# Performance work log

Hardware: AMD Instinct MI355X
Metric: run time of the kernel (lower is better)

Reference implementation:

```python
import jax, jax.numpy as jnp
import numpy as np

N_NODES = 50000
N_EDGES = 1600000


def _gcn_conv(x, src, dst, W, b, num_nodes):
    # PyG GCNConv: out = D^-1/2 (A + I) D^-1/2 (x W) + b
    h = x @ W  # transform first (in_channels >= out_channels)
    deg = jax.ops.segment_sum(jnp.ones_like(dst, dtype=h.dtype), dst,
                              num_segments=num_nodes)
    dinv = jax.lax.rsqrt(deg)  # deg >= 1 thanks to self-loops
    norm = dinv[src] * dinv[dst]  # [E+N]
    msg = h[src] * norm[:, None]  # gather + scale
    out = jax.ops.segment_sum(msg, dst, num_segments=num_nodes)
    return out + b


def setup_inputs() -> dict:
    key = jax.random.key(0)
    k1, k2, k3, k4 = jax.random.split(key, 4)
    x = jax.random.normal(k1, (N_NODES, 512), dtype=jnp.float32)
    edge_index = jax.random.randint(k2, (2, N_EDGES), 0, N_NODES, dtype=jnp.int64)
    # Glorot-ish init for the two GCNConv weights
    W1 = jax.random.normal(k3, (512, 128), dtype=jnp.float32) * (1.0 / np.sqrt(512))
    b1 = jnp.zeros((128,), dtype=jnp.float32)
    W2 = jax.random.normal(k4, (128, 64), dtype=jnp.float32) * (1.0 / np.sqrt(128))
    b2 = jnp.zeros((64,), dtype=jnp.float32)
    return {"x": x, "edge_index": edge_index, "W1": W1, "b1": b1,
            "W2": W2, "b2": b2}


def reference(x, edge_index, W1, b1, W2, b2):
    num_nodes = x.shape[0]
    loop = jnp.arange(num_nodes, dtype=edge_index.dtype)
    src = jnp.concatenate([edge_index[0], loop])  # add self-loops
    dst = jnp.concatenate([edge_index[1], loop])
    h = jax.nn.relu(_gcn_conv(x, src, dst, W1, b1, num_nodes))
    out = _gcn_conv(h, src, dst, W2, b2, num_nodes)
    return out
```

## Files before the change

### kernel.cpp

```cpp
#include <hip/hip_runtime.h>
#include <hip/hip_bf16.h>


typedef __attribute__((ext_vector_type(8))) short short8;
typedef __attribute__((ext_vector_type(4))) float f32x4;

#define BSHIFT 9
#define BSIZE 512
constexpr int NBMAX = 128;
constexpr int CAP = 32768;
constexpr int CHUNK = 4096;

__device__ __forceinline__ unsigned short bf16_bits(float f) {
  __hip_bfloat16 h = __float2bfloat16(f);
  return *(unsigned short*)&h;
}
__device__ __forceinline__ float bf16_f(unsigned short u) {
  __hip_bfloat16 h = *(__hip_bfloat16*)&u;
  return __bfloat162float(h);
}
__device__ __forceinline__ void gload_lds16(const void* g, void* l) {
  __builtin_amdgcn_global_load_lds(
      (const __attribute__((address_space(1))) unsigned*)g,
      (__attribute__((address_space(3))) unsigned*)l, 16, 0, 0);
}
__device__ __forceinline__ int edge_at(const void* p, long long i, int is64) {
  return is64 ? (int)((const long long*)p)[i] : ((const int*)p)[i];
}

__global__ __launch_bounds__(256) void k_binA(
    const void* __restrict__ eidx, int* __restrict__ ccur,
    unsigned* __restrict__ pairs,
    const float* __restrict__ W1, unsigned short* __restrict__ W1h,
    unsigned short* __restrict__ W1l,
    const float* __restrict__ W2, unsigned short* __restrict__ W2h,
    unsigned short* __restrict__ W2l, int E, int NB, int nchunks) {
  const int tid = threadIdx.x;
  if ((int)blockIdx.x >= nchunks) {
    int o = ((int)blockIdx.x - nchunks) * 256 + tid;
    const float* W; unsigned short *Wh, *Wl; int K, Nn;
    if (o < 512 * 128) { W = W1; Wh = W1h; Wl = W1l; K = 512; Nn = 128; }
    else { o -= 512 * 128; if (o >= 128 * 64) return;
           W = W2; Wh = W2h; Wl = W2l; K = 128; Nn = 64; }
    int n = o / K, k = o % K;
    float w = W[(long long)k * Nn + n];
    unsigned short hb = bf16_bits(w);
    Wh[o] = hb;
    Wl[o] = bf16_bits(w - bf16_f(hb));
    return;
  }
  __shared__ int s_nz;
  __shared__ int cnt[NBMAX];
  __shared__ int scn[NBMAX + 1];
  __shared__ int cur[NBMAX];
  __shared__ int gbase[NBMAX];
  __shared__ unsigned out[CHUNK];
  if (tid == 0) s_nz = 0;
  for (int b = tid; b < NBMAX; b += 256) cnt[b] = 0;
  __syncthreads();
  {
    int nz = 0;
    for (int i = 1 + 2 * tid; i < 4096; i += 512)
      nz |= (((const int*)eidx)[i] != 0);
    if (nz) atomicOr(&s_nz, 1);
  }
  __syncthreads();
  const int is64 = (s_nz == 0) ? 1 : 0;
  const int cs = blockIdx.x * CHUNK;
  const int n = min(CHUNK, E - cs);
  unsigned pk[CHUNK / 256];
#pragma unroll
  for (int it = 0; it < CHUNK / 256; ++it) {
    int i = cs + it * 256 + tid;
    unsigned p = 0xFFFFFFFFu;
    if (i < E) {
      int s = edge_at(eidx, i, is64);
      int d = edge_at(eidx, (long long)E + i, is64);
      p = ((unsigned)d << 16) | (unsigned)s;
      atomicAdd(&cnt[d >> BSHIFT], 1);
    }
    pk[it] = p;
  }
  __syncthreads();
  if (tid < NB) scn[tid + 1] = cnt[tid];
  if (tid == 0) scn[0] = 0;
  __syncthreads();
  for (int off = 1; off < NB; off <<= 1) {
    int t = 0;
    if (tid < NB && tid + 1 > off) t = scn[tid + 1 - off];
    __syncthreads();
    if (tid < NB && tid + 1 > off) scn[tid + 1] += t;
    __syncthreads();
  }
  if (tid < NB) {
    cur[tid] = scn[tid];
    gbase[tid] = (cnt[tid] > 0)
        ? (tid * CAP + atomicAdd(&ccur[tid], cnt[tid])) : 0;
  }
  __syncthreads();
#pragma unroll
  for (int it = 0; it < CHUNK / 256; ++it) {
    unsigned p = pk[it];
    if (p != 0xFFFFFFFFu) {
      int b = (int)(p >> (16 + BSHIFT));
      int pos = atomicAdd(&cur[b], 1);
      out[pos] = p;
    }
  }
  __syncthreads();
  for (int p2 = tid; p2 < n; p2 += 256) {
    unsigned v = out[p2];
    int b = (int)(v >> (16 + BSHIFT));
    pairs[gbase[b] + (p2 - scn[b])] = v;
  }
}

__global__ __launch_bounds__(256) void k_binB(
    const unsigned* __restrict__ pairs, const int* __restrict__ ccur,
    int* __restrict__ rowptr, float* __restrict__ dinv,
    unsigned short* __restrict__ elist, int N, int NB, int E) {
  __shared__ int scn2[NBMAX];
  __shared__ int hist[BSIZE];
  __shared__ int loc[BSIZE];
  const int b = blockIdx.x;
  const int tid = threadIdx.x;
  if (b == 0 && tid == 0) rowptr[N] = E;
  if (tid < NBMAX) scn2[tid] = (tid < NB) ? ccur[tid] : 0;
  __syncthreads();
  for (int off = 1; off < NBMAX; off <<= 1) {
    int t = (tid < NBMAX && tid >= off) ? scn2[tid - off] : 0;
    __syncthreads();
    if (tid < NBMAX) scn2[tid] += t;
    __syncthreads();
  }
  const int cntb = ccur[b];
  const int base = scn2[b] - cntb;
  const int nbeg = b * CAP;
  const int j0 = tid, j1 = tid + 256;
  hist[j0] = 0; hist[j1] = 0;
  __syncthreads();
  for (int i = tid; i < cntb; i += 256) {
    unsigned v = pairs[nbeg + i];
    atomicAdd(&hist[(v >> 16) & (BSIZE - 1)], 1);
  }
  __syncthreads();
  loc[j0] = hist[j0]; loc[j1] = hist[j1];
  __syncthreads();
  for (int off = 1; off < BSIZE; off <<= 1) {
    int v0 = (j0 >= off) ? loc[j0 - off] : 0;
    int v1 = (j1 >= off) ? loc[j1 - off] : 0;
    __syncthreads();
    loc[j0] += v0; loc[j1] += v1;
    __syncthreads();
  }
  int c0 = base + loc[j0] - hist[j0];
  int c1 = base + loc[j1] - hist[j1];
  int gd0 = b * BSIZE + j0, gd1 = b * BSIZE + j1;
  if (gd0 < N) { rowptr[gd0] = c0; dinv[gd0] = rsqrtf((float)(hist[j0] + 1)); }
  if (gd1 < N) { rowptr[gd1] = c1; dinv[gd1] = rsqrtf((float)(hist[j1] + 1)); }
  __syncthreads();
  hist[j0] = c0; hist[j1] = c1;
  __syncthreads();
  for (int i = tid; i < cntb; i += 256) {
    unsigned v = pairs[nbeg + i];
    int pos = atomicAdd(&hist[(v >> 16) & (BSIZE - 1)], 1);
    elist[pos] = (unsigned short)(v & 0xFFFFu);
  }
}

template <int K, int NOUT, int WM, int WY, int WX>
__global__ __launch_bounds__(256) void k_gemm_mfma(
    const float* __restrict__ X, const unsigned short* __restrict__ Whi,
    const unsigned short* __restrict__ Wlo, const float* __restrict__ dinv,
    unsigned short* __restrict__ Hs, int M) {
  constexpr int BM = WM * WY;
  constexpr int BN = 64 * WX;
  constexpr int KC = 32;
  constexpr int I = WM / 16;
  static_assert(WY * WX == 4, "4 waves");
  static_assert(BN == NOUT, "block covers full N");
  __shared__ unsigned short Ah[BM][KC], Al[BM][KC];
  __shared__ unsigned short Bh[BN][KC], Bl[BN][KC];
  const int tid = threadIdx.x;
  const int lane = tid & 63, wv = tid >> 6;
  const int wy = wv / WX, wx = wv % WX;
  const int fm = lane & 15;
  const int fq = lane >> 4;
  const int base = blockIdx.x * BM;

  f32x4 acc[I][4];
#pragma unroll
  for (int i = 0; i < I; ++i)
#pragma unroll
    for (int j = 0; j < 4; ++j) acc[i][j] = (f32x4){0.f, 0.f, 0.f, 0.f};

  for (int k0 = 0; k0 < K; k0 += KC) {
    __syncthreads();
#pragma unroll
    for (int it = 0; it < BM / 32; ++it) {
      int chunk = tid + it * 256;
      int r = chunk >> 3, c = chunk & 7;
      float4 v = make_float4(0.f, 0.f, 0.f, 0.f);
      if (base + r < M) v = *(const float4*)&X[(long long)(base + r) * K + k0 + c * 4];
      ushort4 hv, lv;
      hv.x = bf16_bits(v.x); lv.x = bf16_bits(v.x - bf16_f(hv.x));
      hv.y = bf16_bits(v.y); lv.y = bf16_bits(v.y - bf16_f(hv.y));
      hv.z = bf16_bits(v.z); lv.z = bf16_bits(v.z - bf16_f(hv.z));
      hv.w = bf16_bits(v.w); lv.w = bf16_bits(v.w - bf16_f(hv.w));
      *(ushort4*)&Ah[r][c * 4] = hv;
      *(ushort4*)&Al[r][c * 4] = lv;
    }
#pragma unroll
    for (int it = 0; it < (BN * 4) / 256; ++it) {
      int cb = it * 256 + wv * 64;
      int chunk = cb + lane;
      int n = chunk >> 2, cc = chunk & 3;
      const long long go = (long long)n * K + k0 + cc * 8;
      gload_lds16(&Whi[go], (unsigned short*)Bh + (size_t)cb * 8);
      gload_lds16(&Wlo[go], (unsigned short*)Bl + (size_t)cb * 8);
    }
    __syncthreads();
    short8 ah[I], al[I], bh[4], bl[4];
#pragma unroll
    for (int i = 0; i < I; ++i) {
      ah[i] = *(short8*)&Ah[wy * WM + i * 16 + fm][fq * 8];
      al[i] = *(short8*)&Al[wy * WM + i * 16 + fm][fq * 8];
    }
#pragma unroll
    for (int j = 0; j < 4; ++j) {
      bh[j] = *(short8*)&Bh[wx * 64 + j * 16 + fm][fq * 8];
      bl[j] = *(short8*)&Bl[wx * 64 + j * 16 + fm][fq * 8];
    }
#pragma unroll
    for (int i = 0; i < I; ++i)
#pragma unroll
      for (int j = 0; j < 4; ++j) {
        acc[i][j] = __builtin_amdgcn_mfma_f32_16x16x32_bf16(ah[i], bh[j], acc[i][j], 0, 0, 0);
        acc[i][j] = __builtin_amdgcn_mfma_f32_16x16x32_bf16(ah[i], bl[j], acc[i][j], 0, 0, 0);
        acc[i][j] = __builtin_amdgcn_mfma_f32_16x16x32_bf16(al[i], bh[j], acc[i][j], 0, 0, 0);
      }
  }
#pragma unroll
  for (int i = 0; i < I; ++i) {
#pragma unroll
    for (int reg = 0; reg < 4; ++reg) {
      int row = base + wy * WM + i * 16 + fq * 4 + reg;
      if (row < M) {
        float dv = dinv[row];
#pragma unroll
        for (int j = 0; j < 4; ++j)
          Hs[(long long)row * NOUT + wx * 64 + j * 16 + fm] =
              bf16_bits(acc[i][j][reg] * dv);
      }
    }
  }
}

__device__ __forceinline__ void acc8(float* a, uint4 u) {
  const unsigned* p = (const unsigned*)&u;
#pragma unroll
  for (int q = 0; q < 4; ++q) {
    unsigned w = p[q];
    a[2 * q]     += __uint_as_float(w << 16);
    a[2 * q + 1] += __uint_as_float(w & 0xFFFF0000u);
  }
}

template <int C, bool RELU>
__global__ __launch_bounds__(256) void k_gather(
    const int* __restrict__ rowptr, const unsigned short* __restrict__ elist,
    const float* __restrict__ dinv, const unsigned short* __restrict__ Hs,
    const float* __restrict__ bias, float* __restrict__ OUT, int N) {
  constexpr int TPN = C / 8;
  constexpr int NPB = 256 / TPN;
  const int node = blockIdx.x * NPB + (int)threadIdx.x / TPN;
  const int lane = (int)threadIdx.x % TPN;
  if (node >= N) return;
  const int col = lane * 8;
  const int beg = rowptr[node];
  const int end = rowptr[node + 1];
  float a0[8] = {0, 0, 0, 0, 0, 0, 0, 0};
  float a1[8] = {0, 0, 0, 0, 0, 0, 0, 0};
  acc8(a0, *(const uint4*)&Hs[(long long)node * C + col]);
  int e = beg;
  for (; e + 3 < end; e += 4) {
    int s0 = elist[e], s1 = elist[e + 1], s2 = elist[e + 2], s3 = elist[e + 3];
    uint4 v0 = *(const uint4*)&Hs[(long long)s0 * C + col];
    uint4 v1 = *(const uint4*)&Hs[(long long)s1 * C + col];
    uint4 v2 = *(const uint4*)&Hs[(long long)s2 * C + col];
    uint4 v3 = *(const uint4*)&Hs[(long long)s3 * C + col];
    acc8(a0, v0); acc8(a1, v1); acc8(a0, v2); acc8(a1, v3);
  }
  for (; e < end; ++e) {
    uint4 v0 = *(const uint4*)&Hs[(long long)elist[e] * C + col];
    acc8(a0, v0);
  }
  const float dv = dinv[node];
  float o[8];
#pragma unroll
  for (int i = 0; i < 8; ++i) {
    o[i] = (a0[i] + a1[i]) * dv + bias[col + i];
    if (RELU) o[i] = fmaxf(o[i], 0.f);
  }
  *(float4*)&OUT[(long long)node * C + col] = make_float4(o[0], o[1], o[2], o[3]);
  *(float4*)&OUT[(long long)node * C + col + 4] = make_float4(o[4], o[5], o[6], o[7]);
}

extern "C" void kernel_launch(void* const* d_in, const int* in_sizes, int n_in,
                              void* d_out, int out_size, void* d_ws, size_t ws_size,
                              hipStream_t stream) {
  const float* x  = (const float*)d_in[0];
  const void*  ei = d_in[1];
  const float* W1 = (const float*)d_in[2];
  const float* b1 = (const float*)d_in[3];
  const float* W2 = (const float*)d_in[4];
  const float* b2 = (const float*)d_in[5];
  float* out = (float*)d_out;
  const int N = in_sizes[0] / 512;
  const int E = in_sizes[1] / 2;
  const int NB = (N + BSIZE - 1) >> BSHIFT;
  const int nchunks = (E + CHUNK - 1) / CHUNK;

  char* ws = (char*)d_ws;
  size_t off = 0;
  auto take = [&](size_t bytes) {
    void* p = ws + off;
    off = (off + bytes + 255) & ~(size_t)255;
    return p;
  };
  float* dinv   = (float*)take((size_t)N * 4);
  int*   rowptr = (int*)take((size_t)(N + 1) * 4);
  int*   ccur   = (int*)take((size_t)NBMAX * 4);
  unsigned short* elist = (unsigned short*)take((size_t)E * 2);
  unsigned short* Wt1h = (unsigned short*)take((size_t)512 * 128 * 2);
  unsigned short* Wt1l = (unsigned short*)take((size_t)512 * 128 * 2);
  unsigned short* Wt2h = (unsigned short*)take((size_t)128 * 64 * 2);
  unsigned short* Wt2l = (unsigned short*)take((size_t)128 * 64 * 2);
  unsigned short* Hs = (unsigned short*)take((size_t)N * 128 * 2);
  float* h2     = (float*)take((size_t)N * 128 * 4);
  unsigned short* Hs2 = Hs;
  unsigned* pairs = (unsigned*)h2;

  const int B = 256;
  constexpr int WJOBS = (512 * 128 + 128 * 64) / 256;
  hipMemsetAsync(ccur, 0, (size_t)NBMAX * 4, stream);
  k_binA<<<nchunks + WJOBS, B, 0, stream>>>(ei, ccur, pairs,
                                            W1, Wt1h, Wt1l, W2, Wt2h, Wt2l,
                                            E, NB, nchunks);
  k_binB<<<NB, B, 0, stream>>>(pairs, ccur, rowptr, dinv, elist, N, NB, E);
  k_gemm_mfma<512, 128, 32, 2, 2><<<(N + 63) / 64, B, 0, stream>>>(
      x, Wt1h, Wt1l, dinv, Hs, N);
  k_gather<128, true><<<(N + 15) / 16, B, 0, stream>>>(rowptr, elist, dinv, Hs, b1, h2, N);
  k_gemm_mfma<128, 64, 32, 4, 1><<<(N + 127) / 128, B, 0, stream>>>(
      h2, Wt2h, Wt2l, dinv, Hs2, N);
  k_gather<64, false><<<(N + 31) / 32, B, 0, stream>>>(rowptr, elist, dinv, Hs2, b2, out, N);
}
```

Before: 338.7 us.

## Double-buffer LDS tiles in MFMA GEMM and shrink second GEMM tile

Restructures the split-bf16 MFMA GEMM so that LDS holds two buffers. The next K-chunk's A values are loaded into registers and its B tiles issued via global_load_lds while the current chunk is computed, which needs one barrier per iteration instead of two. The second GEMM's per-wave M tile also shrinks from 32 to 16 rows, doubling its block count for more parallelism. The cost is twice the LDS and extra registers for the prefetched A values, and the overlap is only safe if the async LDS loads have completed by the barrier.

```diff
diff --git a/kernel.cpp b/kernel.cpp
--- a/kernel.cpp
+++ b/kernel.cpp
@@ -177,16 +177,20 @@
   constexpr int BN = 64 * WX;
   constexpr int KC = 32;
   constexpr int I = WM / 16;
+  constexpr int NK = K / KC;
+  constexpr int AIT = BM / 32;
+  constexpr int BIT = (BN * 4) / 256;
   static_assert(WY * WX == 4, "4 waves");
   static_assert(BN == NOUT, "block covers full N");
-  __shared__ unsigned short Ah[BM][KC], Al[BM][KC];
-  __shared__ unsigned short Bh[BN][KC], Bl[BN][KC];
+  __shared__ unsigned short Ah[2][BM][KC], Al[2][BM][KC];
+  __shared__ unsigned short Bh[2][BN][KC], Bl[2][BN][KC];
   const int tid = threadIdx.x;
   const int lane = tid & 63, wv = tid >> 6;
   const int wy = wv / WX, wx = wv % WX;
   const int fm = lane & 15;
   const int fq = lane >> 4;
   const int base = blockIdx.x * BM;
+  const int ar = tid >> 3, ac = tid & 7;
 
   f32x4 acc[I][4];
 #pragma unroll
@@ -194,42 +198,52 @@
 #pragma unroll
     for (int j = 0; j < 4; ++j) acc[i][j] = (f32x4){0.f, 0.f, 0.f, 0.f};
 
-  for (int k0 = 0; k0 < K; k0 += KC) {
-    __syncthreads();
-#pragma unroll
-    for (int it = 0; it < BM / 32; ++it) {
-      int chunk = tid + it * 256;
-      int r = chunk >> 3, c = chunk & 7;
-      float4 v = make_float4(0.f, 0.f, 0.f, 0.f);
-      if (base + r < M) v = *(const float4*)&X[(long long)(base + r) * K + k0 + c * 4];
+  float4 av[AIT];
+
+  auto loadA = [&](int k0) {
+#pragma unroll
+    for (int it = 0; it < AIT; ++it) {
+      int r = ar + it * 32;
+      av[it] = make_float4(0.f, 0.f, 0.f, 0.f);
+      if (base + r < M)
+        av[it] = *(const float4*)&X[(long long)(base + r) * K + k0 + ac * 4];
+    }
+  };
+  auto writeA = [&](int buf) {
+#pragma unroll
+    for (int it = 0; it < AIT; ++it) {
+      int r = ar + it * 32;
       ushort4 hv, lv;
-      hv.x = bf16_bits(v.x); lv.x = bf16_bits(v.x - bf16_f(hv.x));
-      hv.y = bf16_bits(v.y); lv.y = bf16_bits(v.y - bf16_f(hv.y));
-      hv.z = bf16_bits(v.z); lv.z = bf16_bits(v.z - bf16_f(hv.z));
-      hv.w = bf16_bits(v.w); lv.w = bf16_bits(v.w - bf16_f(hv.w));
-      *(ushort4*)&Ah[r][c * 4] = hv;
-      *(ushort4*)&Al[r][c * 4] = lv;
-    }
-#pragma unroll
-    for (int it = 0; it < (BN * 4) / 256; ++it) {
+      hv.x = bf16_bits(av[it].x); lv.x = bf16_bits(av[it].x - bf16_f(hv.x));
+      hv.y = bf16_bits(av[it].y); lv.y = bf16_bits(av[it].y - bf16_f(hv.y));
+      hv.z = bf16_bits(av[it].z); lv.z = bf16_bits(av[it].z - bf16_f(hv.z));
+      hv.w = bf16_bits(av[it].w); lv.w = bf16_bits(av[it].w - bf16_f(hv.w));
+      *(ushort4*)&Ah[buf][r][ac * 4] = hv;
+      *(ushort4*)&Al[buf][r][ac * 4] = lv;
+    }
+  };
+  auto issueB = [&](int k0, int buf) {
+#pragma unroll
+    for (int it = 0; it < BIT; ++it) {
       int cb = it * 256 + wv * 64;
       int chunk = cb + lane;
       int n = chunk >> 2, cc = chunk & 3;
       const long long go = (long long)n * K + k0 + cc * 8;
-      gload_lds16(&Whi[go], (unsigned short*)Bh + (size_t)cb * 8);
-      gload_lds16(&Wlo[go], (unsigned short*)Bl + (size_t)cb * 8);
-    }
-    __syncthreads();
+      gload_lds16(&Whi[go], (unsigned short*)&Bh[buf][0][0] + (size_t)cb * 8);
+      gload_lds16(&Wlo[go], (unsigned short*)&Bl[buf][0][0] + (size_t)cb * 8);
+    }
+  };
+  auto compute = [&](int buf) {
     short8 ah[I], al[I], bh[4], bl[4];
 #pragma unroll
     for (int i = 0; i < I; ++i) {
-      ah[i] = *(short8*)&Ah[wy * WM + i * 16 + fm][fq * 8];
-      al[i] = *(short8*)&Al[wy * WM + i * 16 + fm][fq * 8];
+      ah[i] = *(short8*)&Ah[buf][wy * WM + i * 16 + fm][fq * 8];
+      al[i] = *(short8*)&Al[buf][wy * WM + i * 16 + fm][fq * 8];
     }
 #pragma unroll
     for (int j = 0; j < 4; ++j) {
-      bh[j] = *(short8*)&Bh[wx * 64 + j * 16 + fm][fq * 8];
-      bl[j] = *(short8*)&Bl[wx * 64 + j * 16 + fm][fq * 8];
+      bh[j] = *(short8*)&Bh[buf][wx * 64 + j * 16 + fm][fq * 8];
+      bl[j] = *(short8*)&Bl[buf][wx * 64 + j * 16 + fm][fq * 8];
     }
 #pragma unroll
     for (int i = 0; i < I; ++i)
@@ -239,7 +253,23 @@
         acc[i][j] = __builtin_amdgcn_mfma_f32_16x16x32_bf16(ah[i], bl[j], acc[i][j], 0, 0, 0);
         acc[i][j] = __builtin_amdgcn_mfma_f32_16x16x32_bf16(al[i], bh[j], acc[i][j], 0, 0, 0);
       }
-  }
+  };
+
+  loadA(0);
+  issueB(0, 0);
+  writeA(0);
+  __syncthreads();
+  int cur = 0;
+  for (int t = 0; t < NK - 1; ++t) {
+    loadA((t + 1) * KC);
+    issueB((t + 1) * KC, cur ^ 1);
+    compute(cur);
+    writeA(cur ^ 1);
+    __syncthreads();
+    cur ^= 1;
+  }
+  compute(cur);
+
 #pragma unroll
   for (int i = 0; i < I; ++i) {
 #pragma unroll
@@ -351,7 +381,7 @@
   k_gemm_mfma<512, 128, 32, 2, 2><<<(N + 63) / 64, B, 0, stream>>>(
       x, Wt1h, Wt1l, dinv, Hs, N);
   k_gather<128, true><<<(N + 15) / 16, B, 0, stream>>>(rowptr, elist, dinv, Hs, b1, h2, N);
-  k_gemm_mfma<128, 64, 32, 4, 1><<<(N + 127) / 128, B, 0, stream>>>(
+  k_gemm_mfma<128, 64, 16, 4, 1><<<(N + 63) / 64, B, 0, stream>>>(
       h2, Wt2h, Wt2l, dinv, Hs2, N);
   k_gather<64, false><<<(N + 31) / 32, B, 0, stream>>>(rowptr, elist, dinv, Hs2, b2, out, N);
 }
```

Result: no change. 336.3 us (-0.7%).

## Double-buffer GEMM tiles, load A directly to registers, pre-swizzle weights

Applied to the files above, without the earlier changes.

The MFMA GEMM now loads X rows straight into registers in the MFMA fragment layout and converts them to bf16 hi/lo in registers, which removes the A tile in LDS. The weight tiles are prepacked in fragment order by k_binA and double-buffered in LDS, with the next tile's loads issued before the current tile's MFMAs. This is meant to hide global load latency and cut LDS traffic and barriers. The second GEMM also moves to smaller 64-row blocks for more parallelism. In exchange, register pressure rises from keeping two A buffers in flight.

```diff
diff --git a/kernel.cpp b/kernel.cpp
--- a/kernel.cpp
+++ b/kernel.cpp
@@ -38,11 +38,19 @@
   const int tid = threadIdx.x;
   if ((int)blockIdx.x >= nchunks) {
     int o = ((int)blockIdx.x - nchunks) * 256 + tid;
-    const float* W; unsigned short *Wh, *Wl; int K, Nn;
-    if (o < 512 * 128) { W = W1; Wh = W1h; Wl = W1l; K = 512; Nn = 128; }
+    const float* W; unsigned short *Wh, *Wl; int Nn;
+    if (o < 512 * 128) { W = W1; Wh = W1h; Wl = W1l; Nn = 128; }
     else { o -= 512 * 128; if (o >= 128 * 64) return;
-           W = W2; Wh = W2h; Wl = W2l; K = 128; Nn = 64; }
-    int n = o / K, k = o % K;
+           W = W2; Wh = W2h; Wl = W2l; Nn = 64; }
+    int e = o & 7;
+    int fm = (o >> 3) & 15;
+    int fq = (o >> 7) & 3;
+    int rest = o >> 9;
+    int nt16 = Nn >> 4;
+    int jt = rest % nt16;
+    int t = rest / nt16;
+    int k = t * 32 + fq * 8 + e;
+    int n = jt * 16 + fm;
     float w = W[(long long)k * Nn + n];
     unsigned short hb = bf16_bits(w);
     Wh[o] = hb;
@@ -177,10 +185,11 @@
   constexpr int BN = 64 * WX;
   constexpr int KC = 32;
   constexpr int I = WM / 16;
+  constexpr int NK = K / KC;
+  constexpr int BIT = BN / 64;
   static_assert(WY * WX == 4, "4 waves");
   static_assert(BN == NOUT, "block covers full N");
-  __shared__ unsigned short Ah[BM][KC], Al[BM][KC];
-  __shared__ unsigned short Bh[BN][KC], Bl[BN][KC];
+  __shared__ unsigned short Bh[2][BN * KC], Bl[2][BN * KC];
   const int tid = threadIdx.x;
   const int lane = tid & 63, wv = tid >> 6;
   const int wy = wv / WX, wx = wv % WX;
@@ -194,42 +203,64 @@
 #pragma unroll
     for (int j = 0; j < 4; ++j) acc[i][j] = (f32x4){0.f, 0.f, 0.f, 0.f};
 
-  for (int k0 = 0; k0 < K; k0 += KC) {
-    __syncthreads();
-#pragma unroll
-    for (int it = 0; it < BM / 32; ++it) {
-      int chunk = tid + it * 256;
-      int r = chunk >> 3, c = chunk & 7;
-      float4 v = make_float4(0.f, 0.f, 0.f, 0.f);
-      if (base + r < M) v = *(const float4*)&X[(long long)(base + r) * K + k0 + c * 4];
-      ushort4 hv, lv;
-      hv.x = bf16_bits(v.x); lv.x = bf16_bits(v.x - bf16_f(hv.x));
-      hv.y = bf16_bits(v.y); lv.y = bf16_bits(v.y - bf16_f(hv.y));
-      hv.z = bf16_bits(v.z); lv.z = bf16_bits(v.z - bf16_f(hv.z));
-      hv.w = bf16_bits(v.w); lv.w = bf16_bits(v.w - bf16_f(hv.w));
-      *(ushort4*)&Ah[r][c * 4] = hv;
-      *(ushort4*)&Al[r][c * 4] = lv;
-    }
-#pragma unroll
-    for (int it = 0; it < (BN * 4) / 256; ++it) {
+  float4 av[2][I][2];
+
+  auto loadA = [&](int k0, int pb) {
+#pragma unroll
+    for (int i = 0; i < I; ++i) {
+      int row = base + wy * WM + i * 16 + fm;
+      av[pb][i][0] = make_float4(0.f, 0.f, 0.f, 0.f);
+      av[pb][i][1] = make_float4(0.f, 0.f, 0.f, 0.f);
+      if (row < M) {
+        const float4* p = (const float4*)&X[(long long)row * K + k0 + fq * 8];
+        av[pb][i][0] = p[0];
+        av[pb][i][1] = p[1];
+      }
+    }
+  };
+  auto issueB = [&](int t, int buf) {
+#pragma unroll
+    for (int it = 0; it < BIT; ++it) {
       int cb = it * 256 + wv * 64;
-      int chunk = cb + lane;
-      int n = chunk >> 2, cc = chunk & 3;
-      const long long go = (long long)n * K + k0 + cc * 8;
-      gload_lds16(&Whi[go], (unsigned short*)Bh + (size_t)cb * 8);
-      gload_lds16(&Wlo[go], (unsigned short*)Bl + (size_t)cb * 8);
-    }
-    __syncthreads();
-    short8 ah[I], al[I], bh[4], bl[4];
-#pragma unroll
-    for (int i = 0; i < I; ++i) {
-      ah[i] = *(short8*)&Ah[wy * WM + i * 16 + fm][fq * 8];
-      al[i] = *(short8*)&Al[wy * WM + i * 16 + fm][fq * 8];
-    }
+      size_t so = (size_t)t * (BN * 32) + (size_t)(cb + lane) * 8;
+      gload_lds16(&Whi[so], (unsigned short*)&Bh[buf][0] + (size_t)cb * 8);
+      gload_lds16(&Wlo[so], (unsigned short*)&Bl[buf][0] + (size_t)cb * 8);
+    }
+  };
+  auto cvt8 = [&](const float4& a, const float4& b, short8& h, short8& l) {
+    float f0 = a.x, f1 = a.y, f2 = a.z, f3 = a.w;
+    float f4 = b.x, f5 = b.y, f6 = b.z, f7 = b.w;
+    unsigned short hb;
+    hb = bf16_bits(f0); h[0] = (short)hb; l[0] = (short)bf16_bits(f0 - bf16_f(hb));
+    hb = bf16_bits(f1); h[1] = (short)hb; l[1] = (short)bf16_bits(f1 - bf16_f(hb));
+    hb = bf16_bits(f2); h[2] = (short)hb; l[2] = (short)bf16_bits(f2 - bf16_f(hb));
+    hb = bf16_bits(f3); h[3] = (short)hb; l[3] = (short)bf16_bits(f3 - bf16_f(hb));
+    hb = bf16_bits(f4); h[4] = (short)hb; l[4] = (short)bf16_bits(f4 - bf16_f(hb));
+    hb = bf16_bits(f5); h[5] = (short)hb; l[5] = (short)bf16_bits(f5 - bf16_f(hb));
+    hb = bf16_bits(f6); h[6] = (short)hb; l[6] = (short)bf16_bits(f6 - bf16_f(hb));
+    hb = bf16_bits(f7); h[7] = (short)hb; l[7] = (short)bf16_bits(f7 - bf16_f(hb));
+  };
+
+  issueB(0, 0);
+  loadA(0, 0);
+  __syncthreads();
+
+#pragma unroll 2
+  for (int t = 0; t < NK; ++t) {
+    const int pb = t & 1;
+    if (t + 1 < NK) {
+      issueB(t + 1, (t + 1) & 1);
+      loadA((t + 1) * KC, (t + 1) & 1);
+    }
+    short8 ah[I], al[I];
+#pragma unroll
+    for (int i = 0; i < I; ++i) cvt8(av[pb][i][0], av[pb][i][1], ah[i], al[i]);
+    short8 bh[4], bl[4];
 #pragma unroll
     for (int j = 0; j < 4; ++j) {
-      bh[j] = *(short8*)&Bh[wx * 64 + j * 16 + fm][fq * 8];
-      bl[j] = *(short8*)&Bl[wx * 64 + j * 16 + fm][fq * 8];
+      int jt = wx * 4 + j;
+      bh[j] = *(const short8*)&Bh[pb][jt * 512 + lane * 8];
+      bl[j] = *(const short8*)&Bl[pb][jt * 512 + lane * 8];
     }
 #pragma unroll
     for (int i = 0; i < I; ++i)
@@ -239,7 +270,9 @@
         acc[i][j] = __builtin_amdgcn_mfma_f32_16x16x32_bf16(ah[i], bl[j], acc[i][j], 0, 0, 0);
         acc[i][j] = __builtin_amdgcn_mfma_f32_16x16x32_bf16(al[i], bh[j], acc[i][j], 0, 0, 0);
       }
-  }
+    __syncthreads();
+  }
+
 #pragma unroll
   for (int i = 0; i < I; ++i) {
 #pragma unroll
@@ -351,7 +384,7 @@
   k_gemm_mfma<512, 128, 32, 2, 2><<<(N + 63) / 64, B, 0, stream>>>(
       x, Wt1h, Wt1l, dinv, Hs, N);
   k_gather<128, true><<<(N + 15) / 16, B, 0, stream>>>(rowptr, elist, dinv, Hs, b1, h2, N);
-  k_gemm_mfma<128, 64, 32, 4, 1><<<(N + 127) / 128, B, 0, stream>>>(
+  k_gemm_mfma<128, 64, 16, 4, 1><<<(N + 63) / 64, B, 0, stream>>>(
       h2, Wt2h, Wt2l, dinv, Hs2, N);
   k_gather<64, false><<<(N + 31) / 32, B, 0, stream>>>(rowptr, elist, dinv, Hs2, b2, out, N);
 }
```

New measurement: 337.7 us. About the same (-0.3%).
